# Optimization experiments

Hardware: AMD Instinct MI355X
Metric: run time of the kernel (lower is better)

The kernel has to match this reference:

```python
import jax, jax.numpy as jnp
import numpy as np

N, D, H = 4096, 1024, 16
GAMMA = 1.0


def setup_inputs() -> dict:
    key = jax.random.key(0)
    ks = jax.random.split(key, 10)
    s = 1.0 / np.sqrt(D)
    return {
        "x": jax.random.normal(ks[0], (N, D), jnp.float32),
        "h": jax.random.normal(ks[1], (N,), jnp.float32),
        "Wq": jax.random.normal(ks[2], (D, D), jnp.float32) * s,
        "bq": jax.random.normal(ks[3], (D,), jnp.float32) * s,
        "Wk": jax.random.normal(ks[4], (D, D), jnp.float32) * s,
        "bk": jax.random.normal(ks[5], (D,), jnp.float32) * s,
        "Wv": jax.random.normal(ks[6], (D, D), jnp.float32) * s,
        "bv": jax.random.normal(ks[7], (D,), jnp.float32) * s,
        "Wo": jax.random.normal(ks[8], (D, D), jnp.float32) * s,
        "bo": jax.random.normal(ks[9], (D,), jnp.float32) * s,
    }


def reference(x, h, Wq, bq, Wk, bk, Wv, bv, Wo, bo):
    n, d = x.shape
    d_head = d // H
    # torch Linear: y = x @ W.T + b
    q = (x @ Wq.T + bq).reshape(n, H, d_head)
    k = (x @ Wk.T + bk).reshape(n, H, d_head)
    v = (x @ Wv.T + bv).reshape(n, H, d_head)
    scale = 1.0 / np.sqrt(d_head).astype(np.float32)
    logits = jnp.einsum('nhd,mhd->hnm', q, k) * scale  # (H, n, n)
    logits = logits - (GAMMA * h)[None, None, :]       # per-key additive bias
    attn = jax.nn.softmax(logits, axis=-1)
    out = jnp.einsum('hnm,mhd->nhd', attn, v).reshape(n, d)
    return out @ Wo.T + bo + x
```

## Files before the change

### kernel.cpp

```cpp
#include <hip/hip_runtime.h>
#include <hip/hip_bf16.h>
#include <stdint.h>

#define NTOK 4096
#define DM   1024
#define NH   16
#define DH   64
#define SCL  0.1803368801111129f
#define LOG2E 1.4426950408889634f

typedef __attribute__((ext_vector_type(8)))  short bf16x8;
typedef __attribute__((ext_vector_type(4)))  float f32x4;
typedef __attribute__((ext_vector_type(16))) float f32x16;
typedef __attribute__((ext_vector_type(4)))  unsigned short us4;

__device__ inline unsigned short f2bf(float f) {
  union { float f; unsigned int u; } a;
  a.f = f;
  unsigned int u = a.u;
  u += 0x7fffu + ((u >> 16) & 1u);
  return (unsigned short)(u >> 16);
}

__device__ inline unsigned int cvtpk_bf16(float lo, float hi) {
  unsigned int r;
  asm("v_cvt_pk_bf16_f32 %0, %1, %2" : "=v"(r) : "v"(lo), "v"(hi));
  return r;
}

__device__ inline void gload_lds16(const void* gsrc, void* ldst) {
  __builtin_amdgcn_global_load_lds(
      (const __attribute__((address_space(1))) void*)(uintptr_t)gsrc,
      (__attribute__((address_space(3))) void*)(unsigned int)(uintptr_t)ldst,
      16, 0, 0);
}

__global__ void cvt_fused(const float* __restrict__ x,
                          const float* __restrict__ Wq,
                          const float* __restrict__ Wk,
                          const float* __restrict__ Wv,
                          const float* __restrict__ Wo,
                          const float* __restrict__ h,
                          unsigned short* __restrict__ xb,
                          unsigned short* __restrict__ wqkvb,
                          unsigned short* __restrict__ wob,
                          float* __restrict__ hperm) {
  const int b = blockIdx.x;
  if (b >= 8192) {
    int i = (b - 8192) * 256 + threadIdx.x;
    int r  = i & 15;
    int hh = (i >> 4) & 1;
    int t  = i >> 5;
    int key = t * 32 + (r & 3) + 8 * (r >> 2) + 4 * hh;
    hperm[i] = -LOG2E * h[key];
    return;
  }
  int i = b * 256 + threadIdx.x;
  const float* src; unsigned short* dst; int off;
  if (i < 1048576)      { src = x;  dst = xb;                 off = i; }
  else if (i < 1310720) { src = Wq; dst = wqkvb;              off = i - 1048576; }
  else if (i < 1572864) { src = Wk; dst = wqkvb + DM * DM;    off = i - 1310720; }
  else if (i < 1835008) { src = Wv; dst = wqkvb + 2 * DM * DM; off = i - 1572864; }
  else                  { src = Wo; dst = wob;                off = i - 1835008; }
  float4 v = ((const float4*)src)[off];
  us4 o;
  o[0] = f2bf(v.x); o[1] = f2bf(v.y); o[2] = f2bf(v.z); o[3] = f2bf(v.w);
  ((us4*)dst)[off] = o;
}

__global__ __launch_bounds__(256)
void gemm_qkv(const unsigned short* __restrict__ A,
              const unsigned short* __restrict__ B,
              const float* __restrict__ bq, const float* __restrict__ bk,
              const float* __restrict__ bv,
              unsigned short* __restrict__ Qb, unsigned short* __restrict__ Kb,
              unsigned short* __restrict__ Vt)
{
  const int tid  = threadIdx.x;
  const int wid  = tid >> 6;
  const int lane = tid & 63;
  const int bn = blockIdx.x * 128;
  const int bm = blockIdx.y * 128;
  const int wr = wid >> 1;
  const int wc = wid & 1;

  __shared__ __align__(16) unsigned short As[128 * 32];
  __shared__ __align__(16) unsigned short Bs[128 * 32];

  f32x4 acc[4][4];
#pragma unroll
  for (int i = 0; i < 4; i++)
#pragma unroll
    for (int j = 0; j < 4; j++) acc[i][j] = f32x4{0.f, 0.f, 0.f, 0.f};

  const int fr = lane & 15;
  const int fk = (lane >> 4) * 8;
  const int srow = lane >> 2;
  const int scol = (lane & 3) * 8;

  for (int k0 = 0; k0 < DM; k0 += 32) {
#pragma unroll
    for (int c = 0; c < 2; ++c) {
      const int chunk = wid * 2 + c;
      gload_lds16(A + (size_t)(bm + chunk * 16 + srow) * DM + k0 + scol,
                  &As[chunk * 512]);
      gload_lds16(B + (size_t)(bn + chunk * 16 + srow) * DM + k0 + scol,
                  &Bs[chunk * 512]);
    }
    __syncthreads();
    bf16x8 af[4], bfr[4];
#pragma unroll
    for (int i = 0; i < 4; i++)
      af[i] = *(const bf16x8*)&As[(wr * 64 + i * 16 + fr) * 32 + fk];
#pragma unroll
    for (int j = 0; j < 4; j++)
      bfr[j] = *(const bf16x8*)&Bs[(wc * 64 + j * 16 + fr) * 32 + fk];
#pragma unroll
    for (int i = 0; i < 4; i++)
#pragma unroll
      for (int j = 0; j < 4; j++)
        acc[i][j] = __builtin_amdgcn_mfma_f32_16x16x32_bf16(af[i], bfr[j],
                                                            acc[i][j], 0, 0, 0);
    __syncthreads();
  }

  const int fq = lane >> 4;
  const int region = bn >> 10;
  const float* bias = (region == 0) ? bq : (region == 1) ? bk : bv;
  const float qscale = (region == 0) ? SCL : 1.0f;
  unsigned short* outp = (region == 0) ? Qb : Kb;
#pragma unroll
  for (int j = 0; j < 4; j++) {
    const int col = bn + wc * 64 + j * 16 + fr;
    const int cl  = col & 1023;
    const float bvx = bias[cl];
#pragma unroll
    for (int i = 0; i < 4; i++) {
      const int row0 = bm + wr * 64 + i * 16 + fq * 4;
      if (region < 2) {
#pragma unroll
        for (int r = 0; r < 4; r++)
          outp[(size_t)(row0 + r) * DM + cl] = f2bf((acc[i][j][r] + bvx) * qscale);
      } else {
        us4 pk;
#pragma unroll
        for (int r = 0; r < 4; r++) pk[r] = f2bf(acc[i][j][r] + bvx);
        *(us4*)&Vt[(size_t)cl * NTOK + row0] = pk;
      }
    }
  }
}

__global__ __launch_bounds__(256)
void gemm_out(const unsigned short* __restrict__ A,
              const unsigned short* __restrict__ B,
              const float* __restrict__ bias,
              const float* __restrict__ resid,
              float* __restrict__ Cf)
{
  const int tid  = threadIdx.x;
  const int wid  = tid >> 6;
  const int lane = tid & 63;
  const int bn = blockIdx.x * 64;
  const int bm = blockIdx.y * 128;

  __shared__ __align__(16) unsigned short As[128 * 32];
  __shared__ __align__(16) unsigned short Bs[64 * 32];

  f32x4 acc[2][4];
#pragma unroll
  for (int i = 0; i < 2; i++)
#pragma unroll
    for (int j = 0; j < 4; j++) acc[i][j] = f32x4{0.f, 0.f, 0.f, 0.f};

  const int fr = lane & 15;
  const int fk = (lane >> 4) * 8;
  const int srow = lane >> 2;
  const int scol = (lane & 3) * 8;

  for (int k0 = 0; k0 < DM; k0 += 32) {
#pragma unroll
    for (int c = 0; c < 3; ++c) {
      const int chunk = wid * 3 + c;
      if (chunk < 8) {
        gload_lds16(A + (size_t)(bm + chunk * 16 + srow) * DM + k0 + scol,
                    &As[chunk * 512]);
      } else {
        gload_lds16(B + (size_t)(bn + (chunk - 8) * 16 + srow) * DM + k0 + scol,
                    &Bs[(chunk - 8) * 512]);
      }
    }
    __syncthreads();
    bf16x8 af[2], bfr[4];
#pragma unroll
    for (int i = 0; i < 2; i++)
      af[i] = *(const bf16x8*)&As[(wid * 32 + i * 16 + fr) * 32 + fk];
#pragma unroll
    for (int j = 0; j < 4; j++)
      bfr[j] = *(const bf16x8*)&Bs[(j * 16 + fr) * 32 + fk];
#pragma unroll
    for (int i = 0; i < 2; i++)
#pragma unroll
      for (int j = 0; j < 4; j++)
        acc[i][j] = __builtin_amdgcn_mfma_f32_16x16x32_bf16(af[i], bfr[j],
                                                            acc[i][j], 0, 0, 0);
    __syncthreads();
  }

  const int fq = lane >> 4;
#pragma unroll
  for (int j = 0; j < 4; j++) {
    const int col = bn + j * 16 + fr;
    const float bvx = bias[col];
#pragma unroll
    for (int i = 0; i < 2; i++) {
      const int row0 = bm + wid * 32 + i * 16 + fq * 4;
#pragma unroll
      for (int r = 0; r < 4; r++) {
        const size_t idx = (size_t)(row0 + r) * DM + col;
        Cf[idx] = acc[i][j][r] + bvx + resid[idx];
      }
    }
  }
}

#define MFMA32(a, b, c) __builtin_amdgcn_mfma_f32_32x32x16_bf16(a, b, c, 0, 0, 0)

__global__ __launch_bounds__(512)
void attn_kernel(const unsigned short* __restrict__ Q,
                 const unsigned short* __restrict__ K,
                 const unsigned short* __restrict__ Vt,
                 const float* __restrict__ hperm,
                 unsigned short* __restrict__ O)
{
  const int wgid = (blockIdx.x & 7) * 64 + (blockIdx.x >> 3);
  const int head = wgid >> 5;
  const int qblk = wgid & 31;
  const int tid  = threadIdx.x;
  const int wid  = tid >> 6;
  const int grp  = wid >> 2;
  const int w4   = wid & 3;
  const int lane = tid & 63;
  const int c31  = lane & 31;
  const int hi   = lane >> 5;
  const int qwb  = qblk * 128 + w4 * 32;
  const int k0g  = grp * 2048;

  __shared__ __align__(16) char lds_raw[32768];
  char* kbase = lds_raw + grp * 16384;
  char* vbase = kbase + 8192;

  const int srow = w4 * 4 + (lane >> 4);
  const int ssl  = lane & 15;
  const int kq   = ssl ^ srow;
  const int kkey = srow + 16 * (kq >> 3);
  const unsigned short* kg =
      K + (size_t)(k0g + kkey) * DM + head * DH + (kq & 7) * 8;
  const int vd = (kq >> 2) * 16 + srow;
  const unsigned short* vg =
      Vt + (size_t)(head * DH + vd) * NTOK + k0g + (kq & 3) * 8;

  const int fr15 = c31 & 15;
  const int fkh  = c31 >> 4;
  int koffB[4], voffB[2][2];
#pragma unroll
  for (int f = 0; f < 4; f++)
    koffB[f] = fr15 * 256 + (((fkh * 8 + f * 2 + hi) ^ fr15) << 4);
#pragma unroll
  for (int db = 0; db < 2; db++)
#pragma unroll
    for (int ko = 0; ko < 2; ko++)
      voffB[db][ko] =
          fr15 * 256 + ((((db * 2 + fkh) * 4 + ko * 2 + hi) ^ fr15) << 4);

  const unsigned short* qp = Q + (size_t)(qwb + c31) * DM + head * DH + hi * 8;
  const bf16x8 qf0 = *(const bf16x8*)(qp);
  const bf16x8 qf1 = *(const bf16x8*)(qp + 16);
  const bf16x8 qf2 = *(const bf16x8*)(qp + 32);
  const bf16x8 qf3 = *(const bf16x8*)(qp + 48);

  const unsigned int onesw = (c31 == 0) ? 0x3F803F80u : 0u;
  union { unsigned int u[4]; bf16x8 v; } ONE;
  ONE.u[0] = onesw; ONE.u[1] = onesw; ONE.u[2] = onesw; ONE.u[3] = onesw;

  f32x16 o0, o1, o2;
#pragma unroll
  for (int i = 0; i < 16; i++) { o0[i] = 0.f; o1[i] = 0.f; o2[i] = 0.f; }

  gload_lds16(kg, kbase + w4 * 1024);
  gload_lds16(vg, vbase + w4 * 1024);
  __syncthreads();

  int cur = 0;
  const int NT = 2048 / 32;
  for (int t = 0; t < NT; ++t) {
    if (t + 1 < NT) {
      gload_lds16(kg + (size_t)(t + 1) * 32 * DM,
                  kbase + (cur ^ 1) * 4096 + w4 * 1024);
      gload_lds16(vg + (t + 1) * 32,
                  vbase + (cur ^ 1) * 4096 + w4 * 1024);
    }

    const float* hp = hperm + k0g + t * 32 + hi * 16;
    const float4 b0 = *(const float4*)(hp + 0);
    const float4 b1 = *(const float4*)(hp + 4);
    const float4 b2 = *(const float4*)(hp + 8);
    const float4 b3 = *(const float4*)(hp + 12);

    const char* Kb = kbase + cur * 4096;
    const char* Vb = vbase + cur * 4096;
    const bf16x8 kf0 = *(const bf16x8*)(Kb + koffB[0]);
    const bf16x8 kf1 = *(const bf16x8*)(Kb + koffB[1]);
    const bf16x8 kf2 = *(const bf16x8*)(Kb + koffB[2]);
    const bf16x8 kf3 = *(const bf16x8*)(Kb + koffB[3]);

    f32x16 s;
    s[0]  = b0.x; s[1]  = b0.y; s[2]  = b0.z; s[3]  = b0.w;
    s[4]  = b1.x; s[5]  = b1.y; s[6]  = b1.z; s[7]  = b1.w;
    s[8]  = b2.x; s[9]  = b2.y; s[10] = b2.z; s[11] = b2.w;
    s[12] = b3.x; s[13] = b3.y; s[14] = b3.z; s[15] = b3.w;

    s = MFMA32(kf0, qf0, s);
    s = MFMA32(kf1, qf1, s);
    s = MFMA32(kf2, qf2, s);
    s = MFMA32(kf3, qf3, s);

    const bf16x8 v00 = *(const bf16x8*)(Vb + voffB[0][0]);
    const bf16x8 v01 = *(const bf16x8*)(Vb + voffB[0][1]);
    const bf16x8 v10 = *(const bf16x8*)(Vb + voffB[1][0]);
    const bf16x8 v11 = *(const bf16x8*)(Vb + voffB[1][1]);

    float ps[16];
#pragma unroll
    for (int r = 0; r < 16; r++) ps[r] = __builtin_amdgcn_exp2f(s[r]);

    unsigned int X1 = cvtpk_bf16(ps[0],  ps[1]);
    unsigned int X2 = cvtpk_bf16(ps[2],  ps[3]);
    unsigned int Y1 = cvtpk_bf16(ps[4],  ps[5]);
    unsigned int Y2 = cvtpk_bf16(ps[6],  ps[7]);
    asm("v_permlane32_swap_b32 %0, %1" : "+v"(X1), "+v"(Y1));
    asm("v_permlane32_swap_b32 %0, %1" : "+v"(X2), "+v"(Y2));
    unsigned int X3 = cvtpk_bf16(ps[8],  ps[9]);
    unsigned int X4 = cvtpk_bf16(ps[10], ps[11]);
    unsigned int Y3 = cvtpk_bf16(ps[12], ps[13]);
    unsigned int Y4 = cvtpk_bf16(ps[14], ps[15]);
    asm("v_permlane32_swap_b32 %0, %1" : "+v"(X3), "+v"(Y3));
    asm("v_permlane32_swap_b32 %0, %1" : "+v"(X4), "+v"(Y4));

    union { unsigned int u[4]; bf16x8 v; } P0, P1;
    P0.u[0] = X1; P0.u[1] = X2; P0.u[2] = Y1; P0.u[3] = Y2;
    P1.u[0] = X3; P1.u[1] = X4; P1.u[2] = Y3; P1.u[3] = Y4;

    o0 = MFMA32(v00, P0.v, o0);
    o0 = MFMA32(v01, P1.v, o0);
    o1 = MFMA32(v10, P0.v, o1);
    o1 = MFMA32(v11, P1.v, o1);
    o2 = MFMA32(ONE.v, P0.v, o2);
    o2 = MFMA32(ONE.v, P1.v, o2);

    __syncthreads();
    cur ^= 1;
  }

  float l = o2[0];
  l += __shfl_xor(l, 32, 64);

  float* mo = (float*)lds_raw;
  float* mL = (float*)(lds_raw + 17408);
  float* row = &mo[(w4 * 64 + lane) * 17];
#pragma unroll
  for (int half = 0; half < 2; half++) {
    __syncthreads();
    if (grp == 1) {
      const f32x16& hA = half ? o1 : o0;
#pragma unroll
      for (int i = 0; i < 16; i++) row[i] = hA[i];
      if (half == 0 && hi == 0) mL[w4 * 32 + c31] = l;
    }
    __syncthreads();
    if (grp == 0) {
      f32x16& hA = half ? o1 : o0;
#pragma unroll
      for (int i = 0; i < 16; i++) hA[i] += row[i];
      if (half == 0) l += mL[w4 * 32 + c31];
    }
  }

  if (grp == 0) {
    const float inv = 1.0f / l;
    unsigned short* ob = O + (size_t)(qwb + c31) * DM + head * DH;
#pragma unroll
    for (int g = 0; g < 4; g++) {
      us4 pk;
      pk[0] = f2bf(o0[4 * g + 0] * inv); pk[1] = f2bf(o0[4 * g + 1] * inv);
      pk[2] = f2bf(o0[4 * g + 2] * inv); pk[3] = f2bf(o0[4 * g + 3] * inv);
      *(us4*)(ob + 8 * g + 4 * hi) = pk;
      pk[0] = f2bf(o1[4 * g + 0] * inv); pk[1] = f2bf(o1[4 * g + 1] * inv);
      pk[2] = f2bf(o1[4 * g + 2] * inv); pk[3] = f2bf(o1[4 * g + 3] * inv);
      *(us4*)(ob + 32 + 8 * g + 4 * hi) = pk;
    }
  }
}

extern "C" void kernel_launch(void* const* d_in, const int* in_sizes, int n_in,
                              void* d_out, int out_size, void* d_ws, size_t ws_size,
                              hipStream_t stream) {
  const float* x  = (const float*)d_in[0];
  const float* h  = (const float*)d_in[1];
  const float* Wq = (const float*)d_in[2];
  const float* bq = (const float*)d_in[3];
  const float* Wk = (const float*)d_in[4];
  const float* bk = (const float*)d_in[5];
  const float* Wv = (const float*)d_in[6];
  const float* bv = (const float*)d_in[7];
  const float* Wo = (const float*)d_in[8];
  const float* bo = (const float*)d_in[9];
  float* out = (float*)d_out;

  char* ws = (char*)d_ws;
  const size_t MB = 1 << 20;
  unsigned short* xb    = (unsigned short*)(ws + 0 * MB);
  unsigned short* wqkvb = (unsigned short*)(ws + 8 * MB);
  unsigned short* wob   = (unsigned short*)(ws + 14 * MB);
  unsigned short* Qb    = (unsigned short*)(ws + 16 * MB);
  unsigned short* Kb    = (unsigned short*)(ws + 24 * MB);
  unsigned short* Vtb   = (unsigned short*)(ws + 32 * MB);
  unsigned short* AOb   = (unsigned short*)(ws + 40 * MB);
  float*          hperm = (float*)(ws + 48 * MB);

  cvt_fused<<<8208, 256, 0, stream>>>(x, Wq, Wk, Wv, Wo, h,
                                      xb, wqkvb, wob, hperm);

  gemm_qkv<<<dim3(24, 32), 256, 0, stream>>>(xb, wqkvb, bq, bk, bv, Qb, Kb, Vtb);

  attn_kernel<<<dim3(512), 512, 0, stream>>>(Qb, Kb, Vtb, hperm, AOb);

  gemm_out<<<dim3(DM / 64, NTOK / 128), 256, 0, stream>>>(AOb, wob, bo, x, out);
}
```

Before: 170.4 us.

## Remap GEMM blocks across XCDs and compute softmax row sums with VALU adds

Both GEMM kernels switch to a 1-D grid with a block-index swizzle that hands each of the eight XCDs a contiguous range of output tiles, aiming for better L2 reuse of A/B tiles. In the attention kernel, the extra MFMAs against a ones-vector that produced the softmax denominator are replaced by a scalar sum of the fp32 exponentials, followed by the existing cross-half shuffle. This drops two MFMAs and one 16-wide accumulator per iteration at the cost of 15 VALU adds. The sum now uses unrounded fp32 values instead of the bf16-rounded P, which changes numerics slightly.

```diff
diff --git a/kernel.cpp b/kernel.cpp
--- a/kernel.cpp
+++ b/kernel.cpp
@@ -76,11 +76,13 @@
               unsigned short* __restrict__ Qb, unsigned short* __restrict__ Kb,
               unsigned short* __restrict__ Vt)
 {
+  const int bid = blockIdx.x;
+  const int wg  = (bid & 7) * 96 + (bid >> 3);
+  const int bn  = (wg % 24) * 128;
+  const int bm  = (wg / 24) * 128;
   const int tid  = threadIdx.x;
   const int wid  = tid >> 6;
   const int lane = tid & 63;
-  const int bn = blockIdx.x * 128;
-  const int bm = blockIdx.y * 128;
   const int wr = wid >> 1;
   const int wc = wid & 1;
 
@@ -158,11 +160,13 @@
               const float* __restrict__ resid,
               float* __restrict__ Cf)
 {
+  const int bid = blockIdx.x;
+  const int wg  = (bid & 7) * 64 + (bid >> 3);
+  const int bn  = (wg % 16) * 64;
+  const int bm  = (wg / 16) * 128;
   const int tid  = threadIdx.x;
   const int wid  = tid >> 6;
   const int lane = tid & 63;
-  const int bn = blockIdx.x * 64;
-  const int bm = blockIdx.y * 128;
 
   __shared__ __align__(16) unsigned short As[128 * 32];
   __shared__ __align__(16) unsigned short Bs[64 * 32];
@@ -279,13 +283,10 @@
   const bf16x8 qf2 = *(const bf16x8*)(qp + 32);
   const bf16x8 qf3 = *(const bf16x8*)(qp + 48);
 
-  const unsigned int onesw = (c31 == 0) ? 0x3F803F80u : 0u;
-  union { unsigned int u[4]; bf16x8 v; } ONE;
-  ONE.u[0] = onesw; ONE.u[1] = onesw; ONE.u[2] = onesw; ONE.u[3] = onesw;
-
-  f32x16 o0, o1, o2;
-#pragma unroll
-  for (int i = 0; i < 16; i++) { o0[i] = 0.f; o1[i] = 0.f; o2[i] = 0.f; }
+  f32x16 o0, o1;
+#pragma unroll
+  for (int i = 0; i < 16; i++) { o0[i] = 0.f; o1[i] = 0.f; }
+  float l = 0.f;
 
   gload_lds16(kg, kbase + w4 * 1024);
   gload_lds16(vg, vbase + w4 * 1024);
@@ -333,6 +334,10 @@
     float ps[16];
 #pragma unroll
     for (int r = 0; r < 16; r++) ps[r] = __builtin_amdgcn_exp2f(s[r]);
+    l += (((ps[0] + ps[1]) + (ps[2] + ps[3])) +
+          ((ps[4] + ps[5]) + (ps[6] + ps[7]))) +
+         (((ps[8] + ps[9]) + (ps[10] + ps[11])) +
+          ((ps[12] + ps[13]) + (ps[14] + ps[15])));
 
     unsigned int X1 = cvtpk_bf16(ps[0],  ps[1]);
     unsigned int X2 = cvtpk_bf16(ps[2],  ps[3]);
@@ -355,14 +360,11 @@
     o0 = MFMA32(v01, P1.v, o0);
     o1 = MFMA32(v10, P0.v, o1);
     o1 = MFMA32(v11, P1.v, o1);
-    o2 = MFMA32(ONE.v, P0.v, o2);
-    o2 = MFMA32(ONE.v, P1.v, o2);
 
     __syncthreads();
     cur ^= 1;
   }
 
-  float l = o2[0];
   l += __shfl_xor(l, 32, 64);
 
   float* mo = (float*)lds_raw;
@@ -431,9 +433,9 @@
   cvt_fused<<<8208, 256, 0, stream>>>(x, Wq, Wk, Wv, Wo, h,
                                       xb, wqkvb, wob, hperm);
 
-  gemm_qkv<<<dim3(24, 32), 256, 0, stream>>>(xb, wqkvb, bq, bk, bv, Qb, Kb, Vtb);
+  gemm_qkv<<<768, 256, 0, stream>>>(xb, wqkvb, bq, bk, bv, Qb, Kb, Vtb);
 
   attn_kernel<<<dim3(512), 512, 0, stream>>>(Qb, Kb, Vtb, hperm, AOb);
 
-  gemm_out<<<dim3(DM / 64, NTOK / 128), 256, 0, stream>>>(AOb, wob, bo, x, out);
-}
+  gemm_out<<<512, 256, 0, stream>>>(AOb, wob, bo, x, out);
+}
```

New measurement: 169.5 us. About the same (-0.5%).
